# Performance work log

Measured on AMD Instinct MI355X. Metric: run time of the kernel, lower is better.

The kernel has to match this reference:

```python
import jax, jax.numpy as jnp
import numpy as np


def conv1x1(x, w, b):
    # x: [B,C,H,W], w: [O,C], b: [O] -> [B,O,H,W]
    return jnp.einsum('bchw,oc->bohw', x, w) + b[None, :, None, None]


def setup_inputs() -> dict:
    key = jax.random.key(0)
    ks = jax.random.split(key, 8)
    B, C, H, W = 16, 256, 64, 64
    Cq = C // 8
    x = jax.random.normal(ks[0], (B, C, H, W), dtype=jnp.float32)
    wq = jax.random.normal(ks[1], (Cq, C), dtype=jnp.float32) * (2.0 / C) ** 0.5
    bq = jnp.zeros((Cq,), dtype=jnp.float32)
    wk = jax.random.normal(ks[2], (Cq, C), dtype=jnp.float32) * (2.0 / C) ** 0.5
    bk = jnp.zeros((Cq,), dtype=jnp.float32)
    wv = jax.random.normal(ks[3], (C, C), dtype=jnp.float32) * (2.0 / C) ** 0.5
    bv = jnp.zeros((C,), dtype=jnp.float32)
    gamma = jax.random.normal(ks[4], (1,), dtype=jnp.float32) * 0.1
    return {'x': x, 'wq': wq, 'bq': bq, 'wk': wk, 'bk': bk, 'wv': wv, 'bv': bv, 'gamma': gamma}


def reference(x, wq, bq, wk, bk, wv, bv, gamma):
    B, C, H, W = x.shape
    bH = B // 4
    bW = B // 4  # requires bH*bW == B, i.e. B == 16
    q = conv1x1(x, wq, bq)   # [B, C/8, H, W]
    k = conv1x1(x, wk, bk)   # [B, C/8, H, W]
    v = conv1x1(x, wv, bv)   # [B, C, H, W]
    # batch index b -> grid (h = b // bW, w = b % bW); token feature = flat map
    qg = q.reshape(bH, bW, -1)  # [bH, bW, Dq]
    kg = k.reshape(bH, bW, -1)
    vg = v.reshape(bH, bW, -1)  # [bH, bW, Dv]
    # column ('H') attention with -inf diagonal, row ('W') attention
    eH = jnp.einsum('hwd,gwd->hwg', qg, kg)  # [bH, bW, bH]
    eye = jnp.eye(bH, dtype=bool)[:, None, :]  # mask h == h'
    eH = jnp.where(eye, -jnp.inf, eH)
    eW = jnp.einsum('hwd,hgd->hwg', qg, kg)  # [bH, bW, bW]
    att = jax.nn.softmax(jnp.concatenate([eH, eW], axis=-1), axis=-1)
    aH, aW = att[..., :bH], att[..., bH:]
    oH = jnp.einsum('hwg,gwd->hwd', aH, vg)  # attend down the column
    oW = jnp.einsum('hwg,hgd->hwd', aW, vg)  # attend along the row
    out = (oH + oW).reshape(B, C, H, W)
    return gamma[0] * out + x
```

## Files before the change

### kernel.cpp

```cpp
#include <hip/hip_runtime.h>

#define B_   16
#define C_   256
#define HW_  4096
#define DQK  131072
#define DV   1048576

using bf16x8  = __attribute__((ext_vector_type(8))) __bf16;
using ushort8 = __attribute__((ext_vector_type(8))) unsigned short;
using u16x4   = __attribute__((ext_vector_type(4))) unsigned short;
using f32x4   = __attribute__((ext_vector_type(4))) float;

static __device__ __forceinline__ unsigned short f2bf(float f) {
    union { float f; unsigned u; } v; v.f = f;
    unsigned r = v.u + 0x7FFFu + ((v.u >> 16) & 1u);
    return (unsigned short)(r >> 16);
}
static __device__ __forceinline__ float bf2f(unsigned short h) {
    union { unsigned u; float f; } v; v.u = ((unsigned)h) << 16;
    return v.f;
}

__global__ __launch_bounds__(256) void k_pack(const float* wq, const float* wk, const float* wv,
                                              unsigned short* WhF, unsigned short* WlF, unsigned short* WvF) {
    int idx = blockIdx.x * 256 + threadIdx.x;
    if (idx < 16384) {
        int i = idx;
        int mt = i >> 12, cg = (i >> 7) & 31, ml = (i >> 3) & 15, cl = i & 7;
        int m = mt * 16 + ml, c = cg * 8 + cl;
        float f = (m < 32) ? wq[m * 256 + c] : wk[(m - 32) * 256 + c];
        unsigned short hi = f2bf(f);
        WhF[i] = hi;
        WlF[i] = f2bf(f - bf2f(hi));
    } else {
        int i = idx - 16384;
        int mt = i >> 12, kt = (i >> 7) & 31, lr = (i >> 3) & 15, j = i & 7;
        int m = mt * 16 + lr, c = kt * 8 + j;
        WvF[i] = f2bf(wv[m * 256 + c]);
    }
}

__global__ __launch_bounds__(256) void k_gemm_qk(const unsigned short* __restrict__ WhF,
                                                 const unsigned short* __restrict__ WlF,
                                                 const float* __restrict__ x,
                                                 const float* __restrict__ bq, const float* __restrict__ bk,
                                                 float* __restrict__ QF, float* __restrict__ KF) {
    int b  = blockIdx.y;
    int n0 = blockIdx.x * 64;
    int t = threadIdx.x;
    int lane = t & 63, wid = t >> 6;
    int wm = wid & 1, wn = wid >> 1;
    int lr = lane & 15, kg = lane >> 4;

    const float* xb = x + (size_t)b * DV;
    const unsigned short* Ah0 = WhF + (size_t)(wm * 2) * 4096 + lane * 8;
    const unsigned short* Al0 = WlF + (size_t)(wm * 2) * 4096 + lane * 8;

    f32x4 acc[2][2];
    for (int mi = 0; mi < 2; mi++)
        for (int ni = 0; ni < 2; ni++) acc[mi][ni] = (f32x4){0.f, 0.f, 0.f, 0.f};

    for (int kk = 0; kk < 8; kk++) {
        bf16x8 ah[2], al[2];
        for (int mi = 0; mi < 2; mi++) {
            ah[mi] = *(const bf16x8*)(Ah0 + (size_t)mi * 4096 + kk * 512);
            al[mi] = *(const bf16x8*)(Al0 + (size_t)mi * 4096 + kk * 512);
        }
        bf16x8 bh[2], bl[2];
        int cbase = kk * 32 + kg * 8;
        for (int ni = 0; ni < 2; ni++) {
            const float* xp = xb + (size_t)cbase * HW_ + n0 + wn * 32 + ni * 16 + lr;
            #pragma unroll
            for (int j = 0; j < 8; j++) {
                float v = xp[(size_t)j * HW_];
                __bf16 h = (__bf16)v;
                bh[ni][j] = h;
                bl[ni][j] = (__bf16)(v - (float)h);
            }
        }
        for (int mi = 0; mi < 2; mi++)
            for (int ni = 0; ni < 2; ni++) {
                acc[mi][ni] = __builtin_amdgcn_mfma_f32_16x16x32_bf16(ah[mi], bh[ni], acc[mi][ni], 0, 0, 0);
                acc[mi][ni] = __builtin_amdgcn_mfma_f32_16x16x32_bf16(ah[mi], bl[ni], acc[mi][ni], 0, 0, 0);
                acc[mi][ni] = __builtin_amdgcn_mfma_f32_16x16x32_bf16(al[mi], bh[ni], acc[mi][ni], 0, 0, 0);
            }
    }

    float* dst = (wm == 0) ? QF : KF;
    const float* bias = (wm == 0) ? bq : bk;
    for (int mi = 0; mi < 2; mi++) {
        int mq0 = mi * 16 + kg * 4;
        for (int i = 0; i < 4; i++) {
            int mq = mq0 + i;
            float bs = bias[mq];
            for (int ni = 0; ni < 2; ni++) {
                int n = n0 + wn * 32 + ni * 16 + lr;
                dst[(size_t)b * DQK + (size_t)mq * HW_ + n] = acc[mi][ni][i] + bs;
            }
        }
    }
}

__global__ __launch_bounds__(256) void k_scores2(const float* __restrict__ QF, const float* __restrict__ KF,
                                                 float* __restrict__ Sp) {
    __shared__ float Ql[16][520], Kl[16][520];
    int s = blockIdx.x;
    int m = s >> 3, off = (s & 7) * 512;
    int t = threadIdx.x;
    for (int b = 0; b < 16; b++) {
        const float* qs = QF + (size_t)b * DQK + (size_t)m * HW_ + off;
        const float* ks = KF + (size_t)b * DQK + (size_t)m * HW_ + off;
        Ql[b][t]       = qs[t];
        Ql[b][t + 256] = qs[t + 256];
        Kl[b][t]       = ks[t];
        Kl[b][t + 256] = ks[t + 256];
    }
    __syncthreads();
    int p = t >> 1, h = t & 1;
    int b = p >> 3, j = p & 7;
    int hb = b >> 2, wb = b & 3;
    int bp = (j < 4) ? (j * 4 + wb) : (hb * 4 + (j - 4));
    const f32x4* q4 = (const f32x4*)&Ql[b][h * 256];
    const f32x4* k4 = (const f32x4*)&Kl[bp][h * 256];
    f32x4 a4 = (f32x4){0.f, 0.f, 0.f, 0.f};
    for (int i = 0; i < 64; i++) a4 += q4[i] * k4[i];
    float sres = a4[0] + a4[1] + a4[2] + a4[3];
    sres += __shfl_xor(sres, 1);
    if (h == 0) Sp[(size_t)p * 256 + s] = sres;
}

__global__ void k_softmax2(const float* __restrict__ Sp, const float* __restrict__ gamma,
                           float* __restrict__ Mm) {
    __shared__ float SS[128];
    int t = threadIdx.x;
    const f32x4* s4 = (const f32x4*)(Sp + (size_t)t * 256);
    f32x4 a = (f32x4){0.f, 0.f, 0.f, 0.f};
    for (int i = 0; i < 64; i++) a += s4[i];
    SS[t] = a[0] + a[1] + a[2] + a[3];
    __syncthreads();
    if (t < 16) {
        int b = t, h = b >> 2, w = b & 3;
        float e[8];
        for (int j = 0; j < 8; j++) e[j] = SS[b * 8 + j];
        e[h] = -INFINITY;
        float mx = e[0];
        for (int j = 1; j < 8; j++) mx = fmaxf(mx, e[j]);
        float aa[8], sum = 0.f;
        for (int j = 0; j < 8; j++) { aa[j] = expf(e[j] - mx); sum += aa[j]; }
        float inv = 1.0f / sum;
        float g = gamma[0];
        float row[16];
        for (int c = 0; c < 16; c++) row[c] = 0.f;
        for (int gg = 0; gg < 4; gg++) if (gg != h) row[gg * 4 + w] += aa[gg] * inv;
        for (int gg = 0; gg < 4; gg++) row[h * 4 + gg] += aa[4 + gg] * inv;
        for (int c = 0; c < 16; c++) Mm[b * 16 + c] = row[c] * g;
        Mm[256 + b] = g;
    }
}

__global__ __launch_bounds__(256) void k_mix(const float* __restrict__ Mm, const float* __restrict__ x,
                                             unsigned short* __restrict__ Xm) {
    __shared__ float Ms[256];
    __shared__ unsigned short T[16][32][36];
    int t = threadIdx.x;
    int p0 = blockIdx.x * 32, c0 = blockIdx.y * 32;
    Ms[t] = Mm[t];

    int c_l = t >> 3, p4 = t & 7;
    f32x4 in4[16];
    for (int bp = 0; bp < 16; bp++)
        in4[bp] = *(const f32x4*)(x + (size_t)bp * DV + (size_t)(c0 + c_l) * HW_ + p0 + p4 * 4);
    __syncthreads();
    for (int b = 0; b < 16; b++) {
        int h = b >> 2, w = b & 3;
        f32x4 acc = (f32x4){0.f, 0.f, 0.f, 0.f};
        #pragma unroll
        for (int g = 0; g < 4; g++) {
            if (g != h) acc += Ms[b * 16 + g * 4 + w] * in4[g * 4 + w];
            acc += Ms[b * 16 + h * 4 + g] * in4[h * 4 + g];
        }
        for (int e = 0; e < 4; e++) T[b][p4 * 4 + e][c_l] = f2bf(acc[e]);
    }
    __syncthreads();
    int p_l = t >> 3, cq = t & 7;
    int p = p0 + p_l;
    int c = c0 + cq * 4;
    size_t dst = (size_t)(p >> 4) * 4096 + (size_t)(c >> 3) * 128 + (p & 15) * 8 + (c & 7);
    for (int b = 0; b < 16; b++) {
        u16x4 v = *(const u16x4*)&T[b][p_l][cq * 4];
        *(u16x4*)(Xm + (size_t)b * DV + dst) = v;
    }
}

__global__ __launch_bounds__(256) void k_gemm_v_res(const unsigned short* __restrict__ Wvf,
                                                    const unsigned short* __restrict__ Xmf,
                                                    const float* __restrict__ bv,
                                                    const float* __restrict__ MmRs,
                                                    const float* __restrict__ x,
                                                    float* __restrict__ out) {
    int b  = blockIdx.z;
    int m0 = blockIdx.y * 128;
    int n0 = blockIdx.x * 64;
    int t = threadIdx.x;
    int lane = t & 63, wid = t >> 6;
    int wm = wid >> 1, wn = wid & 1;
    int lr = lane & 15, kg = lane >> 4;

    const unsigned short* Ab = Wvf + (size_t)((m0 >> 4) + wm * 4) * 4096 + lane * 8;
    const unsigned short* Bb = Xmf + (size_t)b * DV + (size_t)((n0 >> 4) + wn * 2) * 4096 + lane * 8;

    f32x4 acc[4][2];
    for (int mi = 0; mi < 4; mi++)
        for (int ni = 0; ni < 2; ni++) acc[mi][ni] = (f32x4){0.f, 0.f, 0.f, 0.f};

    #pragma unroll 4
    for (int kk = 0; kk < 8; kk++) {
        bf16x8 a[4], bb[2];
        for (int mi = 0; mi < 4; mi++) a[mi]  = *(const bf16x8*)(Ab + (size_t)mi * 4096 + kk * 512);
        for (int ni = 0; ni < 2; ni++) bb[ni] = *(const bf16x8*)(Bb + (size_t)ni * 4096 + kk * 512);
        for (int mi = 0; mi < 4; mi++)
            for (int ni = 0; ni < 2; ni++)
                acc[mi][ni] = __builtin_amdgcn_mfma_f32_16x16x32_bf16(a[mi], bb[ni], acc[mi][ni], 0, 0, 0);
    }

    float rs_b = MmRs[256 + b];
    for (int mi = 0; mi < 4; mi++) {
        int mbase = m0 + wm * 64 + mi * 16 + kg * 4;
        for (int i = 0; i < 4; i++) {
            int m = mbase + i;
            float bias = rs_b * bv[m];
            size_t rowoff = (size_t)b * DV + (size_t)m * HW_;
            for (int ni = 0; ni < 2; ni++) {
                int n = n0 + wn * 32 + ni * 16 + lr;
                out[rowoff + n] = acc[mi][ni][i] + bias + x[rowoff + n];
            }
        }
    }
}

extern "C" void kernel_launch(void* const* d_in, const int* in_sizes, int n_in,
                              void* d_out, int out_size, void* d_ws, size_t ws_size,
                              hipStream_t stream) {
    (void)in_sizes; (void)n_in; (void)out_size; (void)ws_size;
    const float* x     = (const float*)d_in[0];
    const float* wq    = (const float*)d_in[1];
    const float* bq    = (const float*)d_in[2];
    const float* wk    = (const float*)d_in[3];
    const float* bk    = (const float*)d_in[4];
    const float* wv    = (const float*)d_in[5];
    const float* bv    = (const float*)d_in[6];
    const float* gamma = (const float*)d_in[7];

    char* ws = (char*)d_ws;
    unsigned short* WhF = (unsigned short*)(ws + 0);
    unsigned short* WlF = (unsigned short*)(ws + 32768);
    unsigned short* WvF = (unsigned short*)(ws + 65536);
    float*          QF  = (float*)(ws + 196608);
    float*          KF  = (float*)(ws + 8585216);
    unsigned short* Xm  = (unsigned short*)(ws + 16973824);
    float*          Sp  = (float*)(ws + 16973824);
    float*          Mm  = (float*)(ws + 0);
    float*          vo  = (float*)d_out;

    k_pack       <<<320, 256, 0, stream>>>(wq, wk, wv, WhF, WlF, WvF);
    k_gemm_qk    <<<dim3(64, 16), 256, 0, stream>>>(WhF, WlF, x, bq, bk, QF, KF);
    k_scores2    <<<256, 256, 0, stream>>>(QF, KF, Sp);
    k_softmax2   <<<1, 128, 0, stream>>>(Sp, gamma, Mm);
    k_mix        <<<dim3(128, 8), 256, 0, stream>>>(Mm, x, Xm);
    k_gemm_v_res <<<dim3(64, 2, 16), 256, 0, stream>>>(WvF, Xm, bv, Mm, x, vo);
}
```

Measured before the change: 91.11 us.

## Fuse QK projection with score computation and V projection with mixing/residual

```diff
diff --git a/kernel.cpp b/kernel.cpp
--- a/kernel.cpp
+++ b/kernel.cpp
@@ -1,15 +1,10 @@
 #include <hip/hip_runtime.h>
 
-#define B_   16
-#define C_   256
 #define HW_  4096
-#define DQK  131072
 #define DV   1048576
 
-using bf16x8  = __attribute__((ext_vector_type(8))) __bf16;
-using ushort8 = __attribute__((ext_vector_type(8))) unsigned short;
-using u16x4   = __attribute__((ext_vector_type(4))) unsigned short;
-using f32x4   = __attribute__((ext_vector_type(4))) float;
+using bf16x8 = __attribute__((ext_vector_type(8))) __bf16;
+using f32x4  = __attribute__((ext_vector_type(4))) float;
 
 static __device__ __forceinline__ unsigned short f2bf(float f) {
     union { float f; unsigned u; } v; v.f = f;
@@ -40,103 +35,123 @@
     }
 }
 
-__global__ __launch_bounds__(256) void k_gemm_qk(const unsigned short* __restrict__ WhF,
+__global__ __launch_bounds__(1024, 4) void k_qks(const unsigned short* __restrict__ WhF,
                                                  const unsigned short* __restrict__ WlF,
                                                  const float* __restrict__ x,
                                                  const float* __restrict__ bq, const float* __restrict__ bk,
-                                                 float* __restrict__ QF, float* __restrict__ KF) {
-    int b  = blockIdx.y;
-    int n0 = blockIdx.x * 64;
+                                                 float* __restrict__ Sp) {
+    __shared__ __align__(16) __bf16 SB[2][16][2][1024];
+    int n0 = blockIdx.x * 16;
     int t = threadIdx.x;
     int lane = t & 63, wid = t >> 6;
-    int wm = wid & 1, wn = wid >> 1;
     int lr = lane & 15, kg = lane >> 4;
-
-    const float* xb = x + (size_t)b * DV;
-    const unsigned short* Ah0 = WhF + (size_t)(wm * 2) * 4096 + lane * 8;
-    const unsigned short* Al0 = WlF + (size_t)(wm * 2) * 4096 + lane * 8;
-
-    f32x4 acc[2][2];
-    for (int mi = 0; mi < 2; mi++)
-        for (int ni = 0; ni < 2; ni++) acc[mi][ni] = (f32x4){0.f, 0.f, 0.f, 0.f};
-
-    for (int kk = 0; kk < 8; kk++) {
-        bf16x8 ah[2], al[2];
-        for (int mi = 0; mi < 2; mi++) {
-            ah[mi] = *(const bf16x8*)(Ah0 + (size_t)mi * 4096 + kk * 512);
-            al[mi] = *(const bf16x8*)(Al0 + (size_t)mi * 4096 + kk * 512);
-        }
-        bf16x8 bh[2], bl[2];
-        int cbase = kk * 32 + kg * 8;
-        for (int ni = 0; ni < 2; ni++) {
-            const float* xp = xb + (size_t)cbase * HW_ + n0 + wn * 32 + ni * 16 + lr;
-            #pragma unroll
-            for (int j = 0; j < 8; j++) {
-                float v = xp[(size_t)j * HW_];
-                __bf16 h = (__bf16)v;
-                bh[ni][j] = h;
-                bl[ni][j] = (__bf16)(v - (float)h);
+    int sn = t & 15, sk = t >> 4;
+    int saddr = ((sk >> 3) * 16 + sn) * 8 + (sk & 7);
+
+    f32x4 acc[4];
+    #pragma unroll
+    for (int mf = 0; mf < 4; mf++) acc[mf] = (f32x4){0.f, 0.f, 0.f, 0.f};
+
+    float xv[16];
+    const float* xs0 = x + (size_t)sk * HW_ + n0 + sn;
+    #pragma unroll
+    for (int bp = 0; bp < 16; bp++) xv[bp] = xs0[(size_t)bp * DV];
+    #pragma unroll
+    for (int bp = 0; bp < 16; bp++) {
+        float v = xv[bp]; __bf16 h = (__bf16)v;
+        SB[0][bp][0][saddr] = h;
+        SB[0][bp][1][saddr] = (__bf16)(v - (float)h);
+    }
+    __syncthreads();
+
+    const unsigned short* Abh = WhF + lane * 8;
+    const unsigned short* Abl = WlF + lane * 8;
+
+    for (int c = 0; c < 4; c++) {
+        int cur = c & 1;
+        if (c < 3) {
+            const float* xp = x + (size_t)((c + 1) * 64 + sk) * HW_ + n0 + sn;
+            #pragma unroll
+            for (int bp = 0; bp < 16; bp++) xv[bp] = xp[(size_t)bp * DV];
+        }
+        #pragma unroll
+        for (int sub = 0; sub < 2; sub++) {
+            int kcg = c * 2 + sub;
+            bf16x8 bh = *(const bf16x8*)&SB[cur][wid][0][sub * 512 + lane * 8];
+            bf16x8 bl = *(const bf16x8*)&SB[cur][wid][1][sub * 512 + lane * 8];
+            #pragma unroll
+            for (int mf = 0; mf < 4; mf++) {
+                bf16x8 ah = *(const bf16x8*)(Abh + mf * 4096 + kcg * 512);
+                bf16x8 al = *(const bf16x8*)(Abl + mf * 4096 + kcg * 512);
+                acc[mf] = __builtin_amdgcn_mfma_f32_16x16x32_bf16(ah, bh, acc[mf], 0, 0, 0);
+                acc[mf] = __builtin_amdgcn_mfma_f32_16x16x32_bf16(ah, bl, acc[mf], 0, 0, 0);
+                acc[mf] = __builtin_amdgcn_mfma_f32_16x16x32_bf16(al, bh, acc[mf], 0, 0, 0);
             }
         }
-        for (int mi = 0; mi < 2; mi++)
-            for (int ni = 0; ni < 2; ni++) {
-                acc[mi][ni] = __builtin_amdgcn_mfma_f32_16x16x32_bf16(ah[mi], bh[ni], acc[mi][ni], 0, 0, 0);
-                acc[mi][ni] = __builtin_amdgcn_mfma_f32_16x16x32_bf16(ah[mi], bl[ni], acc[mi][ni], 0, 0, 0);
-                acc[mi][ni] = __builtin_amdgcn_mfma_f32_16x16x32_bf16(al[mi], bh[ni], acc[mi][ni], 0, 0, 0);
+        if (c < 3) {
+            int nb = cur ^ 1;
+            #pragma unroll
+            for (int bp = 0; bp < 16; bp++) {
+                float v = xv[bp]; __bf16 h = (__bf16)v;
+                SB[nb][bp][0][saddr] = h;
+                SB[nb][bp][1][saddr] = (__bf16)(v - (float)h);
             }
-    }
-
-    float* dst = (wm == 0) ? QF : KF;
-    const float* bias = (wm == 0) ? bq : bk;
-    for (int mi = 0; mi < 2; mi++) {
-        int mq0 = mi * 16 + kg * 4;
+        }
+        __syncthreads();
+    }
+
+    __bf16* F = &SB[0][0][0][0];
+    int b = wid;
+    #pragma unroll
+    for (int mf = 0; mf < 4; mf++) {
+        #pragma unroll
         for (int i = 0; i < 4; i++) {
-            int mq = mq0 + i;
-            float bs = bias[mq];
-            for (int ni = 0; ni < 2; ni++) {
-                int n = n0 + wn * 32 + ni * 16 + lr;
-                dst[(size_t)b * DQK + (size_t)mq * HW_ + n] = acc[mi][ni][i] + bs;
-            }
-        }
-    }
-}
-
-__global__ __launch_bounds__(256) void k_scores2(const float* __restrict__ QF, const float* __restrict__ KF,
-                                                 float* __restrict__ Sp) {
-    __shared__ float Ql[16][520], Kl[16][520];
-    int s = blockIdx.x;
-    int m = s >> 3, off = (s & 7) * 512;
-    int t = threadIdx.x;
-    for (int b = 0; b < 16; b++) {
-        const float* qs = QF + (size_t)b * DQK + (size_t)m * HW_ + off;
-        const float* ks = KF + (size_t)b * DQK + (size_t)m * HW_ + off;
-        Ql[b][t]       = qs[t];
-        Ql[b][t + 256] = qs[t + 256];
-        Kl[b][t]       = ks[t];
-        Kl[b][t + 256] = ks[t + 256];
-    }
-    __syncthreads();
-    int p = t >> 1, h = t & 1;
-    int b = p >> 3, j = p & 7;
-    int hb = b >> 2, wb = b & 3;
-    int bp = (j < 4) ? (j * 4 + wb) : (hb * 4 + (j - 4));
-    const f32x4* q4 = (const f32x4*)&Ql[b][h * 256];
-    const f32x4* k4 = (const f32x4*)&Kl[bp][h * 256];
-    f32x4 a4 = (f32x4){0.f, 0.f, 0.f, 0.f};
-    for (int i = 0; i < 64; i++) a4 += q4[i] * k4[i];
-    float sres = a4[0] + a4[1] + a4[2] + a4[3];
-    sres += __shfl_xor(sres, 1);
-    if (h == 0) Sp[(size_t)p * 256 + s] = sres;
-}
-
-__global__ void k_softmax2(const float* __restrict__ Sp, const float* __restrict__ gamma,
+            int row64 = mf * 16 + kg * 4 + i;
+            float val = acc[mf][i] + ((row64 < 32) ? bq[row64] : bk[row64 - 32]);
+            int qk = row64 >> 5;
+            int r  = row64 & 31;
+            int col = r * 16 + lr;
+            __bf16 h = (__bf16)val;
+            __bf16 l = (__bf16)(val - (float)h);
+            int base = qk * 16384 + ((col >> 3) * 16 + b) * 8 + (col & 7);
+            F[base] = h;
+            F[base + 8192] = l;
+        }
+    }
+    __syncthreads();
+
+    if (wid == 0) {
+        f32x4 S = (f32x4){0.f, 0.f, 0.f, 0.f};
+        #pragma unroll
+        for (int s = 0; s < 16; s++) {
+            bf16x8 qh = *(const bf16x8*)&F[s * 512 + lane * 8];
+            bf16x8 ql = *(const bf16x8*)&F[8192 + s * 512 + lane * 8];
+            bf16x8 kh = *(const bf16x8*)&F[16384 + s * 512 + lane * 8];
+            bf16x8 kl = *(const bf16x8*)&F[24576 + s * 512 + lane * 8];
+            S = __builtin_amdgcn_mfma_f32_16x16x32_bf16(qh, kh, S, 0, 0, 0);
+            S = __builtin_amdgcn_mfma_f32_16x16x32_bf16(qh, kl, S, 0, 0, 0);
+            S = __builtin_amdgcn_mfma_f32_16x16x32_bf16(ql, kh, S, 0, 0, 0);
+        }
+        #pragma unroll
+        for (int i = 0; i < 4; i++) {
+            int bb = kg * 4 + i;
+            int bp = lr;
+            int h = bb >> 2, w = bb & 3;
+            float val = S[i];
+            if ((bp & 3) == w) Sp[(size_t)blockIdx.x * 128 + bb * 8 + (bp >> 2)] = val;
+            if ((bp >> 2) == h) Sp[(size_t)blockIdx.x * 128 + bb * 8 + 4 + (bp & 3)] = val;
+        }
+    }
+}
+
+__global__ void k_softmax3(const float* __restrict__ Sp, const float* __restrict__ gamma,
                            float* __restrict__ Mm) {
     __shared__ float SS[128];
     int t = threadIdx.x;
-    const f32x4* s4 = (const f32x4*)(Sp + (size_t)t * 256);
-    f32x4 a = (f32x4){0.f, 0.f, 0.f, 0.f};
-    for (int i = 0; i < 64; i++) a += s4[i];
-    SS[t] = a[0] + a[1] + a[2] + a[3];
+    float s = 0.f;
+    #pragma unroll 8
+    for (int blk = 0; blk < 256; blk++) s += Sp[(size_t)blk * 128 + t];
+    SS[t] = s;
     __syncthreads();
     if (t < 16) {
         int b = t, h = b >> 2, w = b & 3;
@@ -158,82 +173,72 @@
     }
 }
 
-__global__ __launch_bounds__(256) void k_mix(const float* __restrict__ Mm, const float* __restrict__ x,
-                                             unsigned short* __restrict__ Xm) {
-    __shared__ float Ms[256];
-    __shared__ unsigned short T[16][32][36];
+__global__ __launch_bounds__(1024, 4) void k_fused(const unsigned short* __restrict__ WvF,
+                                                   const float* __restrict__ x,
+                                                   const float* __restrict__ bv,
+                                                   const float* __restrict__ Mm,
+                                                   float* __restrict__ out) {
+    __shared__ __align__(16) __bf16 XB[2][16][1024];
+    int n0 = blockIdx.x * 16;
     int t = threadIdx.x;
-    int p0 = blockIdx.x * 32, c0 = blockIdx.y * 32;
-    Ms[t] = Mm[t];
-
-    int c_l = t >> 3, p4 = t & 7;
-    f32x4 in4[16];
-    for (int bp = 0; bp < 16; bp++)
-        in4[bp] = *(const f32x4*)(x + (size_t)bp * DV + (size_t)(c0 + c_l) * HW_ + p0 + p4 * 4);
-    __syncthreads();
+    int lane = t & 63, wid = t >> 6;
+    int lr = lane & 15, kg = lane >> 4;
+    int sn = t & 15, sk = t >> 4;
+    int saddr = ((sk >> 3) * 16 + sn) * 8 + (sk & 7);
+
+    f32x4 u[16];
+    #pragma unroll
+    for (int b = 0; b < 16; b++) u[b] = (f32x4){0.f, 0.f, 0.f, 0.f};
+
+    float xv[16];
+    const float* xs0 = x + (size_t)sk * HW_ + n0 + sn;
+    #pragma unroll
+    for (int bp = 0; bp < 16; bp++) xv[bp] = xs0[(size_t)bp * DV];
+    #pragma unroll
+    for (int bp = 0; bp < 16; bp++) XB[0][bp][saddr] = (__bf16)xv[bp];
+    __syncthreads();
+
+    const unsigned short* Ab = WvF + (size_t)wid * 4096 + lane * 8;
+
+    for (int c = 0; c < 4; c++) {
+        int cur = c & 1;
+        if (c < 3) {
+            const float* xp = x + (size_t)((c + 1) * 64 + sk) * HW_ + n0 + sn;
+            #pragma unroll
+            for (int bp = 0; bp < 16; bp++) xv[bp] = xp[(size_t)bp * DV];
+        }
+        #pragma unroll
+        for (int sub = 0; sub < 2; sub++) {
+            bf16x8 a = *(const bf16x8*)(Ab + (c * 2 + sub) * 512);
+            #pragma unroll
+            for (int b = 0; b < 16; b++) {
+                bf16x8 bb = *(const bf16x8*)&XB[cur][b][sub * 512 + lane * 8];
+                u[b] = __builtin_amdgcn_mfma_f32_16x16x32_bf16(a, bb, u[b], 0, 0, 0);
+            }
+        }
+        if (c < 3) {
+            int nb = cur ^ 1;
+            #pragma unroll
+            for (int bp = 0; bp < 16; bp++) XB[nb][bp][saddr] = (__bf16)xv[bp];
+        }
+        __syncthreads();
+    }
+
+    #pragma unroll
     for (int b = 0; b < 16; b++) {
         int h = b >> 2, w = b & 3;
-        f32x4 acc = (f32x4){0.f, 0.f, 0.f, 0.f};
+        f32x4 m = (f32x4){0.f, 0.f, 0.f, 0.f};
         #pragma unroll
         for (int g = 0; g < 4; g++) {
-            if (g != h) acc += Ms[b * 16 + g * 4 + w] * in4[g * 4 + w];
-            acc += Ms[b * 16 + h * 4 + g] * in4[h * 4 + g];
-        }
-        for (int e = 0; e < 4; e++) T[b][p4 * 4 + e][c_l] = f2bf(acc[e]);
-    }
-    __syncthreads();
-    int p_l = t >> 3, cq = t & 7;
-    int p = p0 + p_l;
-    int c = c0 + cq * 4;
-    size_t dst = (size_t)(p >> 4) * 4096 + (size_t)(c >> 3) * 128 + (p & 15) * 8 + (c & 7);
-    for (int b = 0; b < 16; b++) {
-        u16x4 v = *(const u16x4*)&T[b][p_l][cq * 4];
-        *(u16x4*)(Xm + (size_t)b * DV + dst) = v;
-    }
-}
-
-__global__ __launch_bounds__(256) void k_gemm_v_res(const unsigned short* __restrict__ Wvf,
-                                                    const unsigned short* __restrict__ Xmf,
-                                                    const float* __restrict__ bv,
-                                                    const float* __restrict__ MmRs,
-                                                    const float* __restrict__ x,
-                                                    float* __restrict__ out) {
-    int b  = blockIdx.z;
-    int m0 = blockIdx.y * 128;
-    int n0 = blockIdx.x * 64;
-    int t = threadIdx.x;
-    int lane = t & 63, wid = t >> 6;
-    int wm = wid >> 1, wn = wid & 1;
-    int lr = lane & 15, kg = lane >> 4;
-
-    const unsigned short* Ab = Wvf + (size_t)((m0 >> 4) + wm * 4) * 4096 + lane * 8;
-    const unsigned short* Bb = Xmf + (size_t)b * DV + (size_t)((n0 >> 4) + wn * 2) * 4096 + lane * 8;
-
-    f32x4 acc[4][2];
-    for (int mi = 0; mi < 4; mi++)
-        for (int ni = 0; ni < 2; ni++) acc[mi][ni] = (f32x4){0.f, 0.f, 0.f, 0.f};
-
-    #pragma unroll 4
-    for (int kk = 0; kk < 8; kk++) {
-        bf16x8 a[4], bb[2];
-        for (int mi = 0; mi < 4; mi++) a[mi]  = *(const bf16x8*)(Ab + (size_t)mi * 4096 + kk * 512);
-        for (int ni = 0; ni < 2; ni++) bb[ni] = *(const bf16x8*)(Bb + (size_t)ni * 4096 + kk * 512);
-        for (int mi = 0; mi < 4; mi++)
-            for (int ni = 0; ni < 2; ni++)
-                acc[mi][ni] = __builtin_amdgcn_mfma_f32_16x16x32_bf16(a[mi], bb[ni], acc[mi][ni], 0, 0, 0);
-    }
-
-    float rs_b = MmRs[256 + b];
-    for (int mi = 0; mi < 4; mi++) {
-        int mbase = m0 + wm * 64 + mi * 16 + kg * 4;
+            if (g != h) m += Mm[b * 16 + g * 4 + w] * u[g * 4 + w];
+            m += Mm[b * 16 + h * 4 + g] * u[h * 4 + g];
+        }
+        float rs = Mm[256 + b];
+        #pragma unroll
         for (int i = 0; i < 4; i++) {
-            int m = mbase + i;
-            float bias = rs_b * bv[m];
-            size_t rowoff = (size_t)b * DV + (size_t)m * HW_;
-            for (int ni = 0; ni < 2; ni++) {
-                int n = n0 + wn * 32 + ni * 16 + lr;
-                out[rowoff + n] = acc[mi][ni][i] + bias + x[rowoff + n];
-            }
+            int mrow = wid * 16 + kg * 4 + i;
+            size_t idx = (size_t)b * DV + (size_t)mrow * HW_ + n0 + lr;
+            out[idx] = m[i] + rs * bv[mrow] + x[idx];
         }
     }
 }
@@ -255,17 +260,12 @@
     unsigned short* WhF = (unsigned short*)(ws + 0);
     unsigned short* WlF = (unsigned short*)(ws + 32768);
     unsigned short* WvF = (unsigned short*)(ws + 65536);
-    float*          QF  = (float*)(ws + 196608);
-    float*          KF  = (float*)(ws + 8585216);
-    unsigned short* Xm  = (unsigned short*)(ws + 16973824);
-    float*          Sp  = (float*)(ws + 16973824);
-    float*          Mm  = (float*)(ws + 0);
+    float*          Sp  = (float*)(ws + 196608);
+    float*          Mm  = (float*)(ws + 327680);
     float*          vo  = (float*)d_out;
 
-    k_pack       <<<320, 256, 0, stream>>>(wq, wk, wv, WhF, WlF, WvF);
-    k_gemm_qk    <<<dim3(64, 16), 256, 0, stream>>>(WhF, WlF, x, bq, bk, QF, KF);
-    k_scores2    <<<256, 256, 0, stream>>>(QF, KF, Sp);
-    k_softmax2   <<<1, 128, 0, stream>>>(Sp, gamma, Mm);
-    k_mix        <<<dim3(128, 8), 256, 0, stream>>>(Mm, x, Xm);
-    k_gemm_v_res <<<dim3(64, 2, 16), 256, 0, stream>>>(WvF, Xm, bv, Mm, x, vo);
-}
+    k_pack     <<<320, 256, 0, stream>>>(wq, wk, wv, WhF, WlF, WvF);
+    k_qks      <<<256, 1024, 0, stream>>>(WhF, WlF, x, bq, bk, Sp);
+    k_softmax3 <<<1, 128, 0, stream>>>(Sp, gamma, Mm);
+    k_fused    <<<256, 1024, 0, stream>>>(WvF, x, bv, Mm, vo);
+}
```

New measurement: 103.2 us. +13.2%, slower.

## Fuse batch-mix and V GEMM by applying mixing after projection

Applied to the files above, without the earlier changes.

```diff
diff --git a/kernel.cpp b/kernel.cpp
--- a/kernel.cpp
+++ b/kernel.cpp
@@ -1,15 +1,11 @@
 #include <hip/hip_runtime.h>
 
-#define B_   16
-#define C_   256
 #define HW_  4096
 #define DQK  131072
 #define DV   1048576
 
-using bf16x8  = __attribute__((ext_vector_type(8))) __bf16;
-using ushort8 = __attribute__((ext_vector_type(8))) unsigned short;
-using u16x4   = __attribute__((ext_vector_type(4))) unsigned short;
-using f32x4   = __attribute__((ext_vector_type(4))) float;
+using bf16x8 = __attribute__((ext_vector_type(8))) __bf16;
+using f32x4  = __attribute__((ext_vector_type(4))) float;
 
 static __device__ __forceinline__ unsigned short f2bf(float f) {
     union { float f; unsigned u; } v; v.f = f;
@@ -158,82 +154,86 @@
     }
 }
 
-__global__ __launch_bounds__(256) void k_mix(const float* __restrict__ Mm, const float* __restrict__ x,
-                                             unsigned short* __restrict__ Xm) {
-    __shared__ float Ms[256];
-    __shared__ unsigned short T[16][32][36];
-    int t = threadIdx.x;
-    int p0 = blockIdx.x * 32, c0 = blockIdx.y * 32;
-    Ms[t] = Mm[t];
-
-    int c_l = t >> 3, p4 = t & 7;
-    f32x4 in4[16];
-    for (int bp = 0; bp < 16; bp++)
-        in4[bp] = *(const f32x4*)(x + (size_t)bp * DV + (size_t)(c0 + c_l) * HW_ + p0 + p4 * 4);
+__global__ __launch_bounds__(1024, 4) void k_fused(const unsigned short* __restrict__ WvF,
+                                                   const float* __restrict__ x,
+                                                   const float* __restrict__ bv,
+                                                   const float* __restrict__ Mm,
+                                                   float* __restrict__ out) {
+    __shared__ __align__(16) __bf16 XB[2][16][1088];
+    int n0 = blockIdx.x * 16;
+    int t = threadIdx.x;
+    int lane = t & 63, wid = t >> 6;
+    int lr = lane & 15, kg = lane >> 4;
+    int n4 = t & 3, sk = (t >> 2) & 63, bpg = t >> 8;
+    int sigr = ((lr & 3) << 2) | (lr >> 2);
+
+    f32x4 u[16];
+    #pragma unroll
+    for (int b = 0; b < 16; b++) u[b] = (f32x4){0.f, 0.f, 0.f, 0.f};
+
+    f32x4 xv[4];
+    #pragma unroll
+    for (int bpi = 0; bpi < 4; bpi++)
+        xv[bpi] = *(const f32x4*)(x + (size_t)(bpg * 4 + bpi) * DV + (size_t)sk * HW_ + n0 + n4 * 4);
+    {
+        int rowoff = (sk >> 3) * 136 + (sk & 7);
+        #pragma unroll
+        for (int bpi = 0; bpi < 4; bpi++) {
+            __bf16* basep = &XB[0][bpg * 4 + bpi][rowoff];
+            #pragma unroll
+            for (int e = 0; e < 4; e++)
+                basep[((e << 2) | n4) * 8] = (__bf16)xv[bpi][e];
+        }
+    }
     __syncthreads();
+
+    for (int c = 0; c < 4; c++) {
+        int cur = c & 1;
+        if (c < 3) {
+            #pragma unroll
+            for (int bpi = 0; bpi < 4; bpi++)
+                xv[bpi] = *(const f32x4*)(x + (size_t)(bpg * 4 + bpi) * DV + (size_t)((c + 1) * 64 + sk) * HW_ + n0 + n4 * 4);
+        }
+        #pragma unroll
+        for (int sub = 0; sub < 2; sub++) {
+            bf16x8 a = *(const bf16x8*)(WvF + (size_t)wid * 4096 + (c * 2 + sub) * 512 + lane * 8);
+            const __bf16* bbase = &XB[cur][0][(sub * 4 + kg) * 136 + sigr * 8];
+            #pragma unroll
+            for (int bp = 0; bp < 16; bp++) {
+                bf16x8 bb = *(const bf16x8*)(bbase + bp * 1088);
+                u[bp] = __builtin_amdgcn_mfma_f32_16x16x32_bf16(a, bb, u[bp], 0, 0, 0);
+            }
+        }
+        if (c < 3) {
+            int nb = cur ^ 1;
+            int rowoff = (sk >> 3) * 136 + (sk & 7);
+            #pragma unroll
+            for (int bpi = 0; bpi < 4; bpi++) {
+                __bf16* basep = &XB[nb][bpg * 4 + bpi][rowoff];
+                #pragma unroll
+                for (int e = 0; e < 4; e++)
+                    basep[((e << 2) | n4) * 8] = (__bf16)xv[bpi][e];
+            }
+        }
+        __syncthreads();
+    }
+
+    int mrow0 = wid * 16 + kg * 4;
+    f32x4 bv4 = (f32x4){bv[mrow0], bv[mrow0 + 1], bv[mrow0 + 2], bv[mrow0 + 3]};
+    #pragma unroll
     for (int b = 0; b < 16; b++) {
         int h = b >> 2, w = b & 3;
-        f32x4 acc = (f32x4){0.f, 0.f, 0.f, 0.f};
+        f32x4 mo = (f32x4){0.f, 0.f, 0.f, 0.f};
         #pragma unroll
         for (int g = 0; g < 4; g++) {
-            if (g != h) acc += Ms[b * 16 + g * 4 + w] * in4[g * 4 + w];
-            acc += Ms[b * 16 + h * 4 + g] * in4[h * 4 + g];
-        }
-        for (int e = 0; e < 4; e++) T[b][p4 * 4 + e][c_l] = f2bf(acc[e]);
-    }
-    __syncthreads();
-    int p_l = t >> 3, cq = t & 7;
-    int p = p0 + p_l;
-    int c = c0 + cq * 4;
-    size_t dst = (size_t)(p >> 4) * 4096 + (size_t)(c >> 3) * 128 + (p & 15) * 8 + (c & 7);
-    for (int b = 0; b < 16; b++) {
-        u16x4 v = *(const u16x4*)&T[b][p_l][cq * 4];
-        *(u16x4*)(Xm + (size_t)b * DV + dst) = v;
-    }
-}
-
-__global__ __launch_bounds__(256) void k_gemm_v_res(const unsigned short* __restrict__ Wvf,
-                                                    const unsigned short* __restrict__ Xmf,
-                                                    const float* __restrict__ bv,
-                                                    const float* __restrict__ MmRs,
-                                                    const float* __restrict__ x,
-                                                    float* __restrict__ out) {
-    int b  = blockIdx.z;
-    int m0 = blockIdx.y * 128;
-    int n0 = blockIdx.x * 64;
-    int t = threadIdx.x;
-    int lane = t & 63, wid = t >> 6;
-    int wm = wid >> 1, wn = wid & 1;
-    int lr = lane & 15, kg = lane >> 4;
-
-    const unsigned short* Ab = Wvf + (size_t)((m0 >> 4) + wm * 4) * 4096 + lane * 8;
-    const unsigned short* Bb = Xmf + (size_t)b * DV + (size_t)((n0 >> 4) + wn * 2) * 4096 + lane * 8;
-
-    f32x4 acc[4][2];
-    for (int mi = 0; mi < 4; mi++)
-        for (int ni = 0; ni < 2; ni++) acc[mi][ni] = (f32x4){0.f, 0.f, 0.f, 0.f};
-
-    #pragma unroll 4
-    for (int kk = 0; kk < 8; kk++) {
-        bf16x8 a[4], bb[2];
-        for (int mi = 0; mi < 4; mi++) a[mi]  = *(const bf16x8*)(Ab + (size_t)mi * 4096 + kk * 512);
-        for (int ni = 0; ni < 2; ni++) bb[ni] = *(const bf16x8*)(Bb + (size_t)ni * 4096 + kk * 512);
-        for (int mi = 0; mi < 4; mi++)
-            for (int ni = 0; ni < 2; ni++)
-                acc[mi][ni] = __builtin_amdgcn_mfma_f32_16x16x32_bf16(a[mi], bb[ni], acc[mi][ni], 0, 0, 0);
-    }
-
-    float rs_b = MmRs[256 + b];
-    for (int mi = 0; mi < 4; mi++) {
-        int mbase = m0 + wm * 64 + mi * 16 + kg * 4;
+            if (g != h) mo += Mm[b * 16 + g * 4 + w] * u[g * 4 + w];
+            mo += Mm[b * 16 + h * 4 + g] * u[h * 4 + g];
+        }
+        mo += Mm[256 + b] * bv4;
+        #pragma unroll
         for (int i = 0; i < 4; i++) {
-            int m = mbase + i;
-            float bias = rs_b * bv[m];
-            size_t rowoff = (size_t)b * DV + (size_t)m * HW_;
-            for (int ni = 0; ni < 2; ni++) {
-                int n = n0 + wn * 32 + ni * 16 + lr;
-                out[rowoff + n] = acc[mi][ni][i] + bias + x[rowoff + n];
-            }
+            size_t idx = (size_t)b * DV + (size_t)(mrow0 + i) * HW_ + n0 + lr;
+            out[idx] = mo[i] + x[idx];
         }
     }
 }
@@ -257,15 +257,13 @@
     unsigned short* WvF = (unsigned short*)(ws + 65536);
     float*          QF  = (float*)(ws + 196608);
     float*          KF  = (float*)(ws + 8585216);
-    unsigned short* Xm  = (unsigned short*)(ws + 16973824);
     float*          Sp  = (float*)(ws + 16973824);
-    float*          Mm  = (float*)(ws + 0);
+    float*          Mm  = (float*)(ws + 17104896);
     float*          vo  = (float*)d_out;
 
-    k_pack       <<<320, 256, 0, stream>>>(wq, wk, wv, WhF, WlF, WvF);
-    k_gemm_qk    <<<dim3(64, 16), 256, 0, stream>>>(WhF, WlF, x, bq, bk, QF, KF);
-    k_scores2    <<<256, 256, 0, stream>>>(QF, KF, Sp);
-    k_softmax2   <<<1, 128, 0, stream>>>(Sp, gamma, Mm);
-    k_mix        <<<dim3(128, 8), 256, 0, stream>>>(Mm, x, Xm);
-    k_gemm_v_res <<<dim3(64, 2, 16), 256, 0, stream>>>(WvF, Xm, bv, Mm, x, vo);
-}
+    k_pack     <<<320, 256, 0, stream>>>(wq, wk, wv, WhF, WlF, WvF);
+    k_gemm_qk  <<<dim3(64, 16), 256, 0, stream>>>(WhF, WlF, x, bq, bk, QF, KF);
+    k_scores2  <<<256, 256, 0, stream>>>(QF, KF, Sp);
+    k_softmax2 <<<1, 128, 0, stream>>>(Sp, gamma, Mm);
+    k_fused    <<<256, 1024, 0, stream>>>(WvF, x, bv, Mm, vo);
+}
```

Measured after the change: 92.91 us. About the same (+2.0%).

## Restructure V GEMM epilogue with lane transpose, vector stores, and full-M blocks

Applied to the files above, without the earlier changes.

```diff
diff --git a/kernel.cpp b/kernel.cpp
--- a/kernel.cpp
+++ b/kernel.cpp
@@ -1,15 +1,11 @@
 #include <hip/hip_runtime.h>
 
-#define B_   16
-#define C_   256
 #define HW_  4096
 #define DQK  131072
 #define DV   1048576
 
-using bf16x8  = __attribute__((ext_vector_type(8))) __bf16;
-using ushort8 = __attribute__((ext_vector_type(8))) unsigned short;
-using u16x4   = __attribute__((ext_vector_type(4))) unsigned short;
-using f32x4   = __attribute__((ext_vector_type(4))) float;
+using bf16x8 = __attribute__((ext_vector_type(8))) __bf16;
+using f32x4  = __attribute__((ext_vector_type(4))) float;
 
 static __device__ __forceinline__ unsigned short f2bf(float f) {
     union { float f; unsigned u; } v; v.f = f;
@@ -19,6 +15,26 @@
 static __device__ __forceinline__ float bf2f(unsigned short h) {
     union { unsigned u; float f; } v; v.u = ((unsigned)h) << 16;
     return v.f;
+}
+
+static __device__ __forceinline__ f32x4 xp4(f32x4 v, bool p0, bool p1) {
+    float e01 = p0 ? v[0] : v[1];
+    float r01 = __shfl_xor(e01, 1);
+    float x0 = p0 ? r01 : v[0];
+    float x1 = p0 ? v[1] : r01;
+    float e23 = p0 ? v[2] : v[3];
+    float r23 = __shfl_xor(e23, 1);
+    float x2 = p0 ? r23 : v[2];
+    float x3 = p0 ? v[3] : r23;
+    float eA = p1 ? x0 : x2;
+    float rA = __shfl_xor(eA, 2);
+    float w0 = p1 ? rA : x0;
+    float w2 = p1 ? x2 : rA;
+    float eB = p1 ? x1 : x3;
+    float rB = __shfl_xor(eB, 2);
+    float w1 = p1 ? rB : x1;
+    float w3 = p1 ? x3 : rB;
+    return (f32x4){w0, w1, w2, w3};
 }
 
 __global__ __launch_bounds__(256) void k_pack(const float* wq, const float* wk, const float* wv,
@@ -162,6 +178,7 @@
                                              unsigned short* __restrict__ Xm) {
     __shared__ float Ms[256];
     __shared__ unsigned short T[16][32][36];
+    using u16x4 = __attribute__((ext_vector_type(4))) unsigned short;
     int t = threadIdx.x;
     int p0 = blockIdx.x * 32, c0 = blockIdx.y * 32;
     Ms[t] = Mm[t];
@@ -192,48 +209,68 @@
     }
 }
 
-__global__ __launch_bounds__(256) void k_gemm_v_res(const unsigned short* __restrict__ Wvf,
-                                                    const unsigned short* __restrict__ Xmf,
+__global__ __launch_bounds__(512) void k_gemm_v_res(const unsigned short* __restrict__ WvF,
+                                                    const unsigned short* __restrict__ XmF,
                                                     const float* __restrict__ bv,
                                                     const float* __restrict__ MmRs,
                                                     const float* __restrict__ x,
                                                     float* __restrict__ out) {
-    int b  = blockIdx.z;
-    int m0 = blockIdx.y * 128;
+    int b  = blockIdx.y;
     int n0 = blockIdx.x * 64;
     int t = threadIdx.x;
     int lane = t & 63, wid = t >> 6;
     int wm = wid >> 1, wn = wid & 1;
     int lr = lane & 15, kg = lane >> 4;
 
-    const unsigned short* Ab = Wvf + (size_t)((m0 >> 4) + wm * 4) * 4096 + lane * 8;
-    const unsigned short* Bb = Xmf + (size_t)b * DV + (size_t)((n0 >> 4) + wn * 2) * 4096 + lane * 8;
+    const unsigned short* Bb = XmF + (size_t)b * DV + (size_t)(blockIdx.x * 4 + wn * 2) * 4096 + lane * 8;
+    const unsigned short* Ab = WvF + (size_t)(wm * 4) * 4096 + lane * 8;
+
+    bf16x8 bfr[8][2];
+    #pragma unroll
+    for (int kk = 0; kk < 8; kk++)
+        #pragma unroll
+        for (int ni = 0; ni < 2; ni++)
+            bfr[kk][ni] = *(const bf16x8*)(Bb + (size_t)ni * 4096 + kk * 512);
 
     f32x4 acc[4][2];
+    #pragma unroll
     for (int mi = 0; mi < 4; mi++)
         for (int ni = 0; ni < 2; ni++) acc[mi][ni] = (f32x4){0.f, 0.f, 0.f, 0.f};
 
-    #pragma unroll 4
+    bf16x8 a[4], an[4];
+    #pragma unroll
+    for (int mi = 0; mi < 4; mi++) a[mi] = *(const bf16x8*)(Ab + (size_t)mi * 4096);
+    #pragma unroll
     for (int kk = 0; kk < 8; kk++) {
-        bf16x8 a[4], bb[2];
-        for (int mi = 0; mi < 4; mi++) a[mi]  = *(const bf16x8*)(Ab + (size_t)mi * 4096 + kk * 512);
-        for (int ni = 0; ni < 2; ni++) bb[ni] = *(const bf16x8*)(Bb + (size_t)ni * 4096 + kk * 512);
+        if (kk < 7) {
+            #pragma unroll
+            for (int mi = 0; mi < 4; mi++)
+                an[mi] = *(const bf16x8*)(Ab + (size_t)mi * 4096 + (kk + 1) * 512);
+        }
+        #pragma unroll
         for (int mi = 0; mi < 4; mi++)
+            #pragma unroll
             for (int ni = 0; ni < 2; ni++)
-                acc[mi][ni] = __builtin_amdgcn_mfma_f32_16x16x32_bf16(a[mi], bb[ni], acc[mi][ni], 0, 0, 0);
-    }
-
-    float rs_b = MmRs[256 + b];
+                acc[mi][ni] = __builtin_amdgcn_mfma_f32_16x16x32_bf16(a[mi], bfr[kk][ni], acc[mi][ni], 0, 0, 0);
+        #pragma unroll
+        for (int mi = 0; mi < 4; mi++) a[mi] = an[mi];
+    }
+
+    float rs = MmRs[256 + b];
+    bool p0 = (lane & 1) != 0, p1 = (lane & 2) != 0;
+    #pragma unroll
     for (int mi = 0; mi < 4; mi++) {
-        int mbase = m0 + wm * 64 + mi * 16 + kg * 4;
-        for (int i = 0; i < 4; i++) {
-            int m = mbase + i;
-            float bias = rs_b * bv[m];
-            size_t rowoff = (size_t)b * DV + (size_t)m * HW_;
-            for (int ni = 0; ni < 2; ni++) {
-                int n = n0 + wn * 32 + ni * 16 + lr;
-                out[rowoff + n] = acc[mi][ni][i] + bias + x[rowoff + n];
-            }
+        int mrow0 = wm * 64 + mi * 16 + kg * 4;
+        f32x4 bvv = *(const f32x4*)(bv + mrow0);
+        int mrow = mrow0 + (lane & 3);
+        #pragma unroll
+        for (int ni = 0; ni < 2; ni++) {
+            f32x4 mo = acc[mi][ni] + rs * bvv;
+            f32x4 w4 = xp4(mo, p0, p1);
+            int nq = n0 + wn * 32 + ni * 16 + (lr >> 2) * 4;
+            size_t g = (size_t)b * DV + (size_t)mrow * HW_ + nq;
+            f32x4 rr = *(const f32x4*)(x + g);
+            __builtin_nontemporal_store(w4 + rr, (f32x4*)(out + g));
         }
     }
 }
@@ -267,5 +304,5 @@
     k_scores2    <<<256, 256, 0, stream>>>(QF, KF, Sp);
     k_softmax2   <<<1, 128, 0, stream>>>(Sp, gamma, Mm);
     k_mix        <<<dim3(128, 8), 256, 0, stream>>>(Mm, x, Xm);
-    k_gemm_v_res <<<dim3(64, 2, 16), 256, 0, stream>>>(WvF, Xm, bv, Mm, x, vo);
-}
+    k_gemm_v_res <<<dim3(64, 16), 512, 0, stream>>>(WvF, Xm, bv, Mm, x, vo);
+}
```

Measured after the change: 91.72 us. Within noise of the previous version (+0.7%).
